# Kernel optimization log

Hardware: AMD Instinct MI355X
Metric: run time of the kernel (lower is better)

## Reference

```python
import jax, jax.numpy as jnp
import numpy as np

EMBED_DIM = 1024
NUM_HEADS = 16
HEAD_DIM = EMBED_DIM // NUM_HEADS
BATCH = 1
SEQ = 4096


def setup_inputs() -> dict:
    key = jax.random.key(0)
    ks = jax.random.split(key, 9)
    s = 1.0 / np.sqrt(EMBED_DIM)
    inp = {
        "x": jax.random.normal(ks[0], (BATCH, SEQ, EMBED_DIM), dtype=jnp.float32),
        "Wq": jax.random.uniform(ks[1], (EMBED_DIM, EMBED_DIM), jnp.float32, -s, s),
        "bq": jax.random.uniform(ks[2], (EMBED_DIM,), jnp.float32, -s, s),
        "Wk": jax.random.uniform(ks[3], (EMBED_DIM, EMBED_DIM), jnp.float32, -s, s),
        "bk": jax.random.uniform(ks[4], (EMBED_DIM,), jnp.float32, -s, s),
        "Wv": jax.random.uniform(ks[5], (EMBED_DIM, EMBED_DIM), jnp.float32, -s, s),
        "bv": jax.random.uniform(ks[6], (EMBED_DIM,), jnp.float32, -s, s),
        "Wo": jax.random.uniform(ks[7], (EMBED_DIM, EMBED_DIM), jnp.float32, -s, s),
        "bo": jax.random.uniform(ks[8], (EMBED_DIM,), jnp.float32, -s, s),
    }
    return inp


def _attention(x, Wq, bq, Wk, bk, Wv, bv, Wo, bo):
    B, S, E = x.shape
    # project and split heads: [B, H, S, D]
    def split_heads(t):
        return t.reshape(B, S, NUM_HEADS, HEAD_DIM).transpose(0, 2, 1, 3)
    q = split_heads(x @ Wq + bq)
    k = split_heads(x @ Wk + bk)
    v = split_heads(x @ Wv + bv)
    scale = 1.0 / np.sqrt(HEAD_DIM).astype(np.float32)
    # scores: [B, H, S, S] (torch code materializes these per query chunk;
    # math is identical computed in one shot)
    scores = jnp.einsum("bhqd,bhkd->bhqk", q, k) * scale
    attn = jax.nn.softmax(scores, axis=-1)  # dropout p=0 -> identity
    out = jnp.einsum("bhqk,bhkd->bhqd", attn, v)
    out = out.transpose(0, 2, 1, 3).reshape(B, S, E)
    return out @ Wo + bo


def reference(x, Wq, bq, Wk, bk, Wv, bv, Wo, bo):
    return _attention(x, Wq, bq, Wk, bk, Wv, bv, Wo, bo)
```

## Files before the change

kernel.cpp:

```cpp
#include <hip/hip_runtime.h>
#include <stdint.h>

typedef __bf16 bf16;
typedef __bf16 bf16x2 __attribute__((ext_vector_type(2)));
typedef __bf16 bf16x8 __attribute__((ext_vector_type(8)));
typedef float f32x4 __attribute__((ext_vector_type(4)));
typedef uint32_t u32x2 __attribute__((ext_vector_type(2)));

#define EMB 1024
#define SEQ 4096
#define NH 16
#define HD 64

__device__ __forceinline__ void glds16(const void* g, void* l) {
    __builtin_amdgcn_global_load_lds(
        (const __attribute__((address_space(1))) uint32_t*)(uintptr_t)g,
        (__attribute__((address_space(3))) uint32_t*)(uintptr_t)l,
        16, 0, 0);
}

union PU { bf16x2 h; uint32_t u; };
__device__ __forceinline__ uint32_t pack_bf16(float a, float b) {
    PU p; p.h = (bf16x2){(bf16)a, (bf16)b}; return p.u;
}

template<int NT>
__device__ __forceinline__ void transpose_tile(const float* in, bf16* out,
                                               int R, int C, int rbase, int cbase,
                                               bf16* tile ) {
    const int t = threadIdx.x;
    constexpr int PASSES = 512 / NT;
#pragma unroll
    for (int p = 0; p < PASSES; ++p) {
        int idx = t + p * NT;
        int r = idx >> 3;
        int seg = idx & 7;
        const float* src = in + (size_t)(rbase + r) * C + cbase + seg * 8;
        f32x4 a = *(const f32x4*)src;
        f32x4 b = *(const f32x4*)(src + 4);
#pragma unroll
        for (int i = 0; i < 4; ++i) {
            tile[r * 81 + seg * 8 + i]     = (bf16)a[i];
            tile[r * 81 + seg * 8 + 4 + i] = (bf16)b[i];
        }
    }
    __syncthreads();
#pragma unroll
    for (int p = 0; p < PASSES; ++p) {
        int idx = t + p * NT;
        int r = idx >> 3;
        int seg = idx & 7;
        bf16x8 v;
#pragma unroll
        for (int i = 0; i < 8; ++i) v[i] = tile[(seg * 8 + i) * 81 + r];
        *(bf16x8*)(out + (size_t)(cbase + r) * R + rbase + seg * 8) = v;
    }
}

__global__ __launch_bounds__(256) void prep_k(const float* __restrict__ W0,
                                              const float* __restrict__ W1,
                                              const float* __restrict__ W2,
                                              bf16* __restrict__ o0,
                                              bf16* __restrict__ o1,
                                              bf16* __restrict__ o2,
                                              const float* __restrict__ x,
                                              bf16* __restrict__ xb) {
    __shared__ bf16 tile[64 * 81];
    if (blockIdx.z < 3) {
        const float* in = blockIdx.z == 0 ? W0 : (blockIdx.z == 1 ? W1 : W2);
        bf16* out = blockIdx.z == 0 ? o0 : (blockIdx.z == 1 ? o1 : o2);
        transpose_tile<256>(in, out, EMB, EMB, blockIdx.y * 64, blockIdx.x * 64, tile);
    } else {
        size_t linear = blockIdx.y * 16 + blockIdx.x;
#pragma unroll
        for (int i = 0; i < 4; ++i) {
            size_t base = linear * 16384 + (size_t)i * 4096 + threadIdx.x * 16;
#pragma unroll
            for (int h = 0; h < 2; ++h) {
                f32x4 a = *(const f32x4*)(x + base + h * 8);
                f32x4 b = *(const f32x4*)(x + base + h * 8 + 4);
                bf16x8 v;
#pragma unroll
                for (int j = 0; j < 4; ++j) { v[j] = (bf16)a[j]; v[4 + j] = (bf16)b[j]; }
                *(bf16x8*)(xb + base + h * 8) = v;
            }
        }
    }
}

__global__ __launch_bounds__(256) void transpose_k(const float* __restrict__ in,
                                                   bf16* __restrict__ out,
                                                   int R, int C) {
    __shared__ bf16 tile[64 * 81];
    transpose_tile<256>(in, out, R, C, blockIdx.y * 64, blockIdx.x * 64, tile);
}

template<bool A_BF16, bool FUSED>
__global__ __launch_bounds__(256, 3) void gemm_m97(
    const void* __restrict__ A,
    const bf16* __restrict__ Wt0, const bf16* __restrict__ Wt1,
    const bf16* __restrict__ Wt2,
    const float* __restrict__ b0, const float* __restrict__ b1,
    const float* __restrict__ b2,
    void* __restrict__ out0, void* __restrict__ out1,
    bf16* __restrict__ outVt) {
    constexpr int SMEM_BYTES = A_BF16 ? (FUSED ? 18432 : 16384) : 24576;
    __shared__ __align__(16) uint8_t smem[SMEM_BYTES];
    float* aF = (float*)smem;
    bf16*  aB = (bf16*)smem;
    bf16*  bL = (bf16*)(smem + (A_BF16 ? 8192 : 16384));

    const int t = threadIdx.x;
    const int lane = t & 63;
    const int wave = t >> 6;
    const int l15 = lane & 15;
    const int quad = lane >> 4;
    const int wrow = (wave >> 1) * 64;
    const int wcol = (wave & 1) * 64;
    const int nb = blockIdx.x;
    const int which = FUSED ? (nb >> 3) : 0;
    const int ncol = (FUSED ? (nb & 7) : nb) * 128;
    const int mblock = blockIdx.y * 128;

    const bf16* Wt = FUSED ? (which == 0 ? Wt0 : (which == 1 ? Wt1 : Wt2)) : Wt0;
    const float* bias = FUSED ? (which == 0 ? b0 : (which == 1 ? b1 : b2)) : b0;

    float bv[4];
#pragma unroll
    for (int nt = 0; nt < 4; ++nt) bv[nt] = bias[ncol + wcol + nt * 16 + l15];

    f32x4 acc[4][4];
#pragma unroll
    for (int mt = 0; mt < 4; ++mt)
#pragma unroll
        for (int nt = 0; nt < 4; ++nt) acc[mt][nt] = (f32x4){0.f, 0.f, 0.f, 0.f};

    const int a4row = lane >> 3, a4seg = lane & 7;
    const int b2row = lane >> 2, b2seg = lane & 3;

    for (int k0 = 0; k0 < EMB; k0 += 32) {
        __syncthreads();
        if constexpr (!A_BF16) {
#pragma unroll
            for (int i = 0; i < 4; ++i) {
                int row = i * 32 + wave * 8 + a4row;
                int sg = a4seg ^ (row & 7);
                glds16((const float*)A + (size_t)(mblock + row) * EMB + k0 + sg * 4,
                       smem + i * 4096 + wave * 1024);
            }
        } else {
#pragma unroll
            for (int i = 0; i < 2; ++i) {
                int row = i * 64 + wave * 16 + b2row;
                int sg = b2seg ^ ((row >> 1) & 3);
                glds16((const bf16*)A + (size_t)(mblock + row) * EMB + k0 + sg * 8,
                       smem + i * 4096 + wave * 1024);
            }
        }
#pragma unroll
        for (int i = 0; i < 2; ++i) {
            int row = i * 64 + wave * 16 + b2row;
            int sg = b2seg ^ ((row >> 1) & 3);
            glds16(Wt + (size_t)(ncol + row) * EMB + k0 + sg * 8,
                   (uint8_t*)bL + i * 4096 + wave * 1024);
        }
        __syncthreads();

        bf16x8 af[4], bfr[4];
#pragma unroll
        for (int mt = 0; mt < 4; ++mt) {
            int rl = wrow + mt * 16 + l15;
            if constexpr (!A_BF16) {
                f32x4 lo = *(const f32x4*)(aF + rl * 32 + ((2 * quad)     ^ (rl & 7)) * 4);
                f32x4 hi = *(const f32x4*)(aF + rl * 32 + ((2 * quad + 1) ^ (rl & 7)) * 4);
#pragma unroll
                for (int j = 0; j < 4; ++j) {
                    af[mt][j]     = (bf16)lo[j];
                    af[mt][4 + j] = (bf16)hi[j];
                }
            } else {
                af[mt] = *(const bf16x8*)(aB + rl * 32 + (quad ^ ((rl >> 1) & 3)) * 8);
            }
        }
#pragma unroll
        for (int nt = 0; nt < 4; ++nt) {
            int rl = wcol + nt * 16 + l15;
            bfr[nt] = *(const bf16x8*)(bL + rl * 32 + (quad ^ ((rl >> 1) & 3)) * 8);
        }
#pragma unroll
        for (int mt = 0; mt < 4; ++mt)
#pragma unroll
            for (int nt = 0; nt < 4; ++nt)
                acc[mt][nt] = __builtin_amdgcn_mfma_f32_16x16x32_bf16(
                    af[mt], bfr[nt], acc[mt][nt], 0, 0, 0);
    }

    if (!FUSED || which < 2) {
        void* outp = FUSED ? (which == 0 ? out0 : out1) : out0;
#pragma unroll
        for (int mt = 0; mt < 4; ++mt)
#pragma unroll
            for (int nt = 0; nt < 4; ++nt)
#pragma unroll
                for (int r = 0; r < 4; ++r) {
                    size_t row = mblock + wrow + mt * 16 + quad * 4 + r;
                    size_t col = ncol + wcol + nt * 16 + l15;
                    float v = acc[mt][nt][r] + bv[nt];
                    if constexpr (FUSED) ((bf16*)outp)[row * EMB + col] = (bf16)v;
                    else                 ((float*)outp)[row * EMB + col] = v;
                }
    } else if constexpr (FUSED) {
        __syncthreads();
        bf16* tr = (bf16*)smem + wave * 2304;
#pragma unroll
        for (int ch = 0; ch < 2; ++ch) {
#pragma unroll
            for (int mt = 0; mt < 4; ++mt)
#pragma unroll
                for (int ntl = 0; ntl < 2; ++ntl)
#pragma unroll
                    for (int r = 0; r < 4; ++r) {
                        int d_local = ntl * 16 + l15;
                        int s_local = mt * 16 + quad * 4 + r;
                        int nt = 2 * ch + ntl;
                        tr[d_local * 72 + s_local] = (bf16)(acc[mt][nt][r] + bv[nt]);
                    }
            int d2 = lane & 31, h2 = lane >> 5;
#pragma unroll
            for (int j = 0; j < 4; ++j) {
                bf16x8 v = *(const bf16x8*)(tr + d2 * 72 + h2 * 32 + j * 8);
                *(bf16x8*)(outVt + (size_t)(ncol + wcol + ch * 32 + d2) * SEQ +
                           mblock + wrow + h2 * 32 + j * 8) = v;
            }
        }
    }
}

__global__ __launch_bounds__(256, 2) void attn_k(bf16* __restrict__ QO,
                                                 const bf16* __restrict__ Km,
                                                 const bf16* __restrict__ Vt,
                                                 const float* __restrict__ Wo,
                                                 bf16* __restrict__ wt_o) {
    __shared__ bf16 k_lds[2][64 * 64];
    __shared__ bf16 v_lds[2][64 * 64];
    __shared__ bf16 p_lds[4][2][16][72];

    if (blockIdx.y == NH) {
        bf16* tile = &k_lds[0][0];
#pragma unroll 1
        for (int i = 0; i < 8; ++i) {
            int tid = blockIdx.x * 8 + i;
            int ty = tid >> 4, tx = tid & 15;
            transpose_tile<256>(Wo, wt_o, EMB, EMB, ty * 64, tx * 64, tile);
            __syncthreads();
        }
        return;
    }

    const int t = threadIdx.x;
    const int lane = t & 63;
    const int wave = t >> 6;
    const int l15 = lane & 15;
    const int quad = lane >> 4;
    const int sw = l15 & 7;
    const int h = blockIdx.y;
    const int qbase = blockIdx.x * 128 + wave * 32;
    const float QSCALE = 0.125f * 1.4426950408889634f;

    const int srow = wave * 16 + (lane >> 3);
    const int ssg  = lane & 7;

    bf16x8 qf[2][2];
#pragma unroll
    for (int qt = 0; qt < 2; ++qt)
#pragma unroll
        for (int kk = 0; kk < 2; ++kk) {
            bf16x8 raw = *(const bf16x8*)(QO + (size_t)(qbase + qt * 16 + l15) * EMB +
                                          h * HD + kk * 32 + quad * 8);
#pragma unroll
            for (int j = 0; j < 8; ++j) qf[qt][kk][j] = (bf16)((float)raw[j] * QSCALE);
        }

    f32x4 o_acc[2][4];
#pragma unroll
    for (int qt = 0; qt < 2; ++qt)
#pragma unroll
        for (int c = 0; c < 4; ++c) o_acc[qt][c] = (f32x4){0.f, 0.f, 0.f, 0.f};
    float l_run[2] = {0.f, 0.f};

#define STAGE(buf, kbv)                                                               \
    do {                                                                              \
        _Pragma("unroll")                                                             \
        for (int i = 0; i < 2; ++i) {                                                 \
            int rr = srow + i * 8;                                                    \
            int sg = ssg ^ (rr & 7);                                                  \
            glds16(Km + (size_t)((kbv) + rr) * EMB + h * HD + sg * 8,                 \
                   &k_lds[buf][(wave * 16 + i * 8) * 64]);                            \
            glds16(Vt + (size_t)(h * HD + rr) * SEQ + (kbv) + sg * 8,                 \
                   &v_lds[buf][(wave * 16 + i * 8) * 64]);                            \
        }                                                                             \
    } while (0)

#define COMPUTE(buf)                                                                  \
    do {                                                                              \
        f32x4 s[2][4];                                                                \
        _Pragma("unroll")                                                             \
        for (int c = 0; c < 4; ++c) {                                                 \
            int row = c * 16 + l15;                                                   \
            bf16x8 k0 = *(const bf16x8*)&k_lds[buf][row * 64 + ((quad)     ^ sw) * 8];\
            bf16x8 k1 = *(const bf16x8*)&k_lds[buf][row * 64 + ((4 + quad) ^ sw) * 8];\
            _Pragma("unroll")                                                         \
            for (int qt = 0; qt < 2; ++qt) {                                          \
                f32x4 z = (f32x4){0.f, 0.f, 0.f, 0.f};                                \
                z = __builtin_amdgcn_mfma_f32_16x16x32_bf16(k0, qf[qt][0], z, 0, 0, 0);\
                s[qt][c] = __builtin_amdgcn_mfma_f32_16x16x32_bf16(k1, qf[qt][1], z, 0, 0, 0);\
            }                                                                         \
        }                                                                             \
        _Pragma("unroll")                                                             \
        for (int qt = 0; qt < 2; ++qt)                                                \
            _Pragma("unroll")                                                         \
            for (int c = 0; c < 4; ++c) {                                             \
                float p0 = __builtin_amdgcn_exp2f(s[qt][c][0]);                       \
                float p1 = __builtin_amdgcn_exp2f(s[qt][c][1]);                       \
                float p2 = __builtin_amdgcn_exp2f(s[qt][c][2]);                       \
                float p3 = __builtin_amdgcn_exp2f(s[qt][c][3]);                       \
                l_run[qt] += (p0 + p1) + (p2 + p3);                                   \
                *(u32x2*)&p_lds[wave][qt][l15][c * 16 + quad * 4] =                   \
                    (u32x2){pack_bf16(p0, p1), pack_bf16(p2, p3)};                    \
            }                                                                         \
        bf16x8 pf[2][2];                                                              \
        _Pragma("unroll")                                                             \
        for (int qt = 0; qt < 2; ++qt)                                                \
            _Pragma("unroll")                                                         \
            for (int tt = 0; tt < 2; ++tt)                                            \
                pf[qt][tt] = *(const bf16x8*)&p_lds[wave][qt][l15][tt * 32 + quad * 8];\
        _Pragma("unroll")                                                             \
        for (int c = 0; c < 4; ++c) {                                                 \
            int row = c * 16 + l15;                                                   \
            bf16x8 v0 = *(const bf16x8*)&v_lds[buf][row * 64 + ((quad)     ^ sw) * 8];\
            bf16x8 v1 = *(const bf16x8*)&v_lds[buf][row * 64 + ((4 + quad) ^ sw) * 8];\
            _Pragma("unroll")                                                         \
            for (int qt = 0; qt < 2; ++qt) {                                          \
                o_acc[qt][c] = __builtin_amdgcn_mfma_f32_16x16x32_bf16(               \
                    pf[qt][0], v0, o_acc[qt][c], 0, 0, 0);                            \
                o_acc[qt][c] = __builtin_amdgcn_mfma_f32_16x16x32_bf16(               \
                    pf[qt][1], v1, o_acc[qt][c], 0, 0, 0);                            \
            }                                                                         \
        }                                                                             \
    } while (0)

    STAGE(0, 0);
    for (int kb = 0; kb < SEQ; kb += 128) {
        __syncthreads();
        STAGE(1, kb + 64);
        COMPUTE(0);
        __syncthreads();
        if (kb + 128 < SEQ) STAGE(0, kb + 128);
        COMPUTE(1);
    }
#undef STAGE
#undef COMPUTE

#pragma unroll
    for (int qt = 0; qt < 2; ++qt) {
        float l = l_run[qt];
        l += __shfl_xor(l, 16);
        l += __shfl_xor(l, 32);
        float inv = 1.0f / l;
#pragma unroll
        for (int r = 0; r < 4; ++r) {
            float invr = __shfl(inv, quad * 4 + r);
#pragma unroll
            for (int c = 0; c < 4; ++c)
                QO[(size_t)(qbase + qt * 16 + quad * 4 + r) * EMB + h * HD + c * 16 + l15] =
                    (bf16)(o_acc[qt][c][r] * invr);
        }
    }
}

extern "C" void kernel_launch(void* const* d_in, const int* in_sizes, int n_in,
                              void* d_out, int out_size, void* d_ws, size_t ws_size,
                              hipStream_t stream) {
    const float* x  = (const float*)d_in[0];
    const float* Wq = (const float*)d_in[1];
    const float* bq = (const float*)d_in[2];
    const float* Wk = (const float*)d_in[3];
    const float* bk = (const float*)d_in[4];
    const float* Wv = (const float*)d_in[5];
    const float* bv = (const float*)d_in[6];
    const float* Wo = (const float*)d_in[7];
    const float* bo = (const float*)d_in[8];

    const size_t MAT = (size_t)SEQ * EMB;
    const size_t WMT = (size_t)EMB * EMB;

    bf16* o16   = (bf16*)d_out;
    bf16* Wt_q  = o16;
    bf16* Wt_k  = o16 + WMT;
    bf16* Wt_v  = o16 + 2 * WMT;
    bf16* Vtb   = o16 + 3 * WMT;

    bf16* wsb   = (bf16*)d_ws;
    bf16* QOb   = wsb;
    bf16* Kb    = wsb + MAT;
    bf16* xb    = wsb + 2 * MAT;

    dim3 blk(256);
    dim3 gP(16, 16, 4);
    dim3 gF(24, SEQ / 128);
    dim3 gO(EMB / 128, SEQ / 128);

    if (ws_size >= 3 * MAT * sizeof(bf16)) {
        prep_k<<<gP, blk, 0, stream>>>(Wq, Wk, Wv, Wt_q, Wt_k, Wt_v, x, xb);

        gemm_m97<true, true><<<gF, blk, 0, stream>>>(
            xb, Wt_q, Wt_k, Wt_v, bq, bk, bv, QOb, Kb, Vtb);

        dim3 gA(SEQ / 128, NH + 1);
        attn_k<<<gA, blk, 0, stream>>>(QOb, Kb, Vtb, Wo, xb);

        gemm_m97<true, false><<<gO, blk, 0, stream>>>(
            QOb, xb, nullptr, nullptr, bo, nullptr, nullptr, d_out, nullptr, nullptr);
    } else {
        bf16* Wt_o = wsb + MAT;
        dim3 gTW(EMB / 64, EMB / 64);
        transpose_k<<<gTW, blk, 0, stream>>>(Wq, Wt_q, EMB, EMB);
        transpose_k<<<gTW, blk, 0, stream>>>(Wk, Wt_k, EMB, EMB);
        transpose_k<<<gTW, blk, 0, stream>>>(Wv, Wt_v, EMB, EMB);
        gemm_m97<false, true><<<gF, blk, 0, stream>>>(
            x, Wt_q, Wt_k, Wt_v, bq, bk, bv, QOb, Kb, Vtb);
        dim3 gA(SEQ / 128, NH);
        attn_k<<<gA, blk, 0, stream>>>(QOb, Kb, Vtb, nullptr, nullptr);
        transpose_k<<<gTW, blk, 0, stream>>>(Wo, Wt_o, EMB, EMB);
        gemm_m97<true, false><<<gO, blk, 0, stream>>>(
            QOb, Wt_o, nullptr, nullptr, bo, nullptr, nullptr, d_out, nullptr, nullptr);
    }
}
```

Before: 234.1 us.

## Switch attention to 32x32x16 MFMA and keep P in registers via permlane32 swap

Replaces the 16x16x32 MFMA tiling in the attention kernel with 32x32x16 MFMAs, computing S^T per 32-key block so the probability fragments can be reshuffled in registers with permlane32_swap instead of round-tripping through a per-wave LDS buffer. This removes the p_lds shared array and its store/load traffic and raises the occupancy hint from 2 to 3 blocks per CU. The output normalization and store are rewritten for the 32x32 accumulator layout. Register pressure from f32x16 accumulators may limit whether the higher occupancy target is reachable.

Result: no change. 232.1 us (-0.9%).

```diff
diff --git a/kernel.cpp b/kernel.cpp
--- a/kernel.cpp
+++ b/kernel.cpp
@@ -5,6 +5,7 @@
 typedef __bf16 bf16x2 __attribute__((ext_vector_type(2)));
 typedef __bf16 bf16x8 __attribute__((ext_vector_type(8)));
 typedef float f32x4 __attribute__((ext_vector_type(4)));
+typedef float f32x16 __attribute__((ext_vector_type(16)));
 typedef uint32_t u32x2 __attribute__((ext_vector_type(2)));
 
 #define EMB 1024
@@ -23,6 +24,7 @@
 __device__ __forceinline__ uint32_t pack_bf16(float a, float b) {
     PU p; p.h = (bf16x2){(bf16)a, (bf16)b}; return p.u;
 }
+union FU { bf16x8 v; uint32_t u[4]; };
 
 template<int NT>
 __device__ __forceinline__ void transpose_tile(const float* in, bf16* out,
@@ -236,14 +238,13 @@
     }
 }
 
-__global__ __launch_bounds__(256, 2) void attn_k(bf16* __restrict__ QO,
+__global__ __launch_bounds__(256, 3) void attn_k(bf16* __restrict__ QO,
                                                  const bf16* __restrict__ Km,
                                                  const bf16* __restrict__ Vt,
                                                  const float* __restrict__ Wo,
                                                  bf16* __restrict__ wt_o) {
     __shared__ bf16 k_lds[2][64 * 64];
     __shared__ bf16 v_lds[2][64 * 64];
-    __shared__ bf16 p_lds[4][2][16][72];
 
     if (blockIdx.y == NH) {
         bf16* tile = &k_lds[0][0];
@@ -260,33 +261,31 @@
     const int t = threadIdx.x;
     const int lane = t & 63;
     const int wave = t >> 6;
-    const int l15 = lane & 15;
-    const int quad = lane >> 4;
-    const int sw = l15 & 7;
-    const int h = blockIdx.y;
+    const int l31 = lane & 31;
+    const int hi = lane >> 5;
+    const int l7 = lane & 7;
+    const int head = blockIdx.y;
     const int qbase = blockIdx.x * 128 + wave * 32;
     const float QSCALE = 0.125f * 1.4426950408889634f;
 
     const int srow = wave * 16 + (lane >> 3);
     const int ssg  = lane & 7;
 
-    bf16x8 qf[2][2];
-#pragma unroll
-    for (int qt = 0; qt < 2; ++qt)
-#pragma unroll
-        for (int kk = 0; kk < 2; ++kk) {
-            bf16x8 raw = *(const bf16x8*)(QO + (size_t)(qbase + qt * 16 + l15) * EMB +
-                                          h * HD + kk * 32 + quad * 8);
-#pragma unroll
-            for (int j = 0; j < 8; ++j) qf[qt][kk][j] = (bf16)((float)raw[j] * QSCALE);
-        }
-
-    f32x4 o_acc[2][4];
-#pragma unroll
-    for (int qt = 0; qt < 2; ++qt)
-#pragma unroll
-        for (int c = 0; c < 4; ++c) o_acc[qt][c] = (f32x4){0.f, 0.f, 0.f, 0.f};
-    float l_run[2] = {0.f, 0.f};
+    bf16x8 qf[4];
+#pragma unroll
+    for (int s = 0; s < 4; ++s) {
+        bf16x8 raw = *(const bf16x8*)(QO + (size_t)(qbase + l31) * EMB +
+                                      head * HD + s * 16 + hi * 8);
+#pragma unroll
+        for (int j = 0; j < 8; ++j) qf[s][j] = (bf16)((float)raw[j] * QSCALE);
+    }
+
+    f32x16 o_acc[2];
+#pragma unroll
+    for (int db = 0; db < 2; ++db)
+#pragma unroll
+        for (int z = 0; z < 16; ++z) o_acc[db][z] = 0.f;
+    float l_run = 0.f;
 
 #define STAGE(buf, kbv)                                                               \
     do {                                                                              \
@@ -294,57 +293,51 @@
         for (int i = 0; i < 2; ++i) {                                                 \
             int rr = srow + i * 8;                                                    \
             int sg = ssg ^ (rr & 7);                                                  \
-            glds16(Km + (size_t)((kbv) + rr) * EMB + h * HD + sg * 8,                 \
+            glds16(Km + (size_t)((kbv) + rr) * EMB + head * HD + sg * 8,              \
                    &k_lds[buf][(wave * 16 + i * 8) * 64]);                            \
-            glds16(Vt + (size_t)(h * HD + rr) * SEQ + (kbv) + sg * 8,                 \
+            glds16(Vt + (size_t)(head * HD + rr) * SEQ + (kbv) + sg * 8,              \
                    &v_lds[buf][(wave * 16 + i * 8) * 64]);                            \
         }                                                                             \
     } while (0)
 
 #define COMPUTE(buf)                                                                  \
     do {                                                                              \
-        f32x4 s[2][4];                                                                \
         _Pragma("unroll")                                                             \
-        for (int c = 0; c < 4; ++c) {                                                 \
-            int row = c * 16 + l15;                                                   \
-            bf16x8 k0 = *(const bf16x8*)&k_lds[buf][row * 64 + ((quad)     ^ sw) * 8];\
-            bf16x8 k1 = *(const bf16x8*)&k_lds[buf][row * 64 + ((4 + quad) ^ sw) * 8];\
+        for (int b = 0; b < 2; ++b) {                                                 \
+            f32x16 sa;                                                               \
             _Pragma("unroll")                                                         \
-            for (int qt = 0; qt < 2; ++qt) {                                          \
-                f32x4 z = (f32x4){0.f, 0.f, 0.f, 0.f};                                \
-                z = __builtin_amdgcn_mfma_f32_16x16x32_bf16(k0, qf[qt][0], z, 0, 0, 0);\
-                s[qt][c] = __builtin_amdgcn_mfma_f32_16x16x32_bf16(k1, qf[qt][1], z, 0, 0, 0);\
+            for (int z = 0; z < 16; ++z) sa[z] = 0.f;                                 \
+            _Pragma("unroll")                                                         \
+            for (int s = 0; s < 4; ++s) {                                             \
+                bf16x8 kf = *(const bf16x8*)&k_lds[buf][(32 * b + l31) * 64 +         \
+                                (((2 * s + hi) ^ l7) * 8)];                           \
+                sa = __builtin_amdgcn_mfma_f32_32x32x16_bf16(kf, qf[s], sa, 0, 0, 0); \
             }                                                                         \
-        }                                                                             \
-        _Pragma("unroll")                                                             \
-        for (int qt = 0; qt < 2; ++qt)                                                \
+            uint32_t u0[4], u1[4];                                                    \
             _Pragma("unroll")                                                         \
-            for (int c = 0; c < 4; ++c) {                                             \
-                float p0 = __builtin_amdgcn_exp2f(s[qt][c][0]);                       \
-                float p1 = __builtin_amdgcn_exp2f(s[qt][c][1]);                       \
-                float p2 = __builtin_amdgcn_exp2f(s[qt][c][2]);                       \
-                float p3 = __builtin_amdgcn_exp2f(s[qt][c][3]);                       \
-                l_run[qt] += (p0 + p1) + (p2 + p3);                                   \
-                *(u32x2*)&p_lds[wave][qt][l15][c * 16 + quad * 4] =                   \
-                    (u32x2){pack_bf16(p0, p1), pack_bf16(p2, p3)};                    \
+            for (int i = 0; i < 4; ++i) {                                             \
+                float p0 = __builtin_amdgcn_exp2f(sa[4 * i + 0]);                     \
+                float p1 = __builtin_amdgcn_exp2f(sa[4 * i + 1]);                     \
+                float p2 = __builtin_amdgcn_exp2f(sa[4 * i + 2]);                     \
+                float p3 = __builtin_amdgcn_exp2f(sa[4 * i + 3]);                     \
+                l_run += (p0 + p1) + (p2 + p3);                                       \
+                u0[i] = pack_bf16(p0, p1);                                            \
+                u1[i] = pack_bf16(p2, p3);                                            \
             }                                                                         \
-        bf16x8 pf[2][2];                                                              \
-        _Pragma("unroll")                                                             \
-        for (int qt = 0; qt < 2; ++qt)                                                \
             _Pragma("unroll")                                                         \
-            for (int tt = 0; tt < 2; ++tt)                                            \
-                pf[qt][tt] = *(const bf16x8*)&p_lds[wave][qt][l15][tt * 32 + quad * 8];\
-        _Pragma("unroll")                                                             \
-        for (int c = 0; c < 4; ++c) {                                                 \
-            int row = c * 16 + l15;                                                   \
-            bf16x8 v0 = *(const bf16x8*)&v_lds[buf][row * 64 + ((quad)     ^ sw) * 8];\
-            bf16x8 v1 = *(const bf16x8*)&v_lds[buf][row * 64 + ((4 + quad) ^ sw) * 8];\
-            _Pragma("unroll")                                                         \
-            for (int qt = 0; qt < 2; ++qt) {                                          \
-                o_acc[qt][c] = __builtin_amdgcn_mfma_f32_16x16x32_bf16(               \
-                    pf[qt][0], v0, o_acc[qt][c], 0, 0, 0);                            \
-                o_acc[qt][c] = __builtin_amdgcn_mfma_f32_16x16x32_bf16(               \
-                    pf[qt][1], v1, o_acc[qt][c], 0, 0, 0);                            \
+            for (int sp = 0; sp < 2; ++sp) {                                          \
+                u32x2 ra = __builtin_amdgcn_permlane32_swap(u0[2 * sp], u0[2 * sp + 1], false, false); \
+                u32x2 rb = __builtin_amdgcn_permlane32_swap(u1[2 * sp], u1[2 * sp + 1], false, false); \
+                FU A;                                                                 \
+                A.u[0] = ra[0]; A.u[1] = rb[0]; A.u[2] = ra[1]; A.u[3] = rb[1];       \
+                int tt = 2 * b + sp;                                                  \
+                _Pragma("unroll")                                                     \
+                for (int db = 0; db < 2; ++db) {                                      \
+                    bf16x8 vf = *(const bf16x8*)&v_lds[buf][(db * 32 + l31) * 64 +    \
+                                    (((2 * tt + hi) ^ l7) * 8)];                      \
+                    o_acc[db] = __builtin_amdgcn_mfma_f32_32x32x16_bf16(              \
+                        A.v, vf, o_acc[db], 0, 0, 0);                                 \
+                }                                                                     \
             }                                                                         \
         }                                                                             \
     } while (0)
@@ -361,21 +354,20 @@
 #undef STAGE
 #undef COMPUTE
 
-#pragma unroll
-    for (int qt = 0; qt < 2; ++qt) {
-        float l = l_run[qt];
-        l += __shfl_xor(l, 16);
-        l += __shfl_xor(l, 32);
-        float inv = 1.0f / l;
-#pragma unroll
-        for (int r = 0; r < 4; ++r) {
-            float invr = __shfl(inv, quad * 4 + r);
-#pragma unroll
-            for (int c = 0; c < 4; ++c)
-                QO[(size_t)(qbase + qt * 16 + quad * 4 + r) * EMB + h * HD + c * 16 + l15] =
-                    (bf16)(o_acc[qt][c][r] * invr);
-        }
-    }
+    l_run += __shfl_xor(l_run, 32);
+    float inv = 1.0f / l_run;
+    float invr[16];
+#pragma unroll
+    for (int reg = 0; reg < 16; ++reg)
+        invr[reg] = __shfl(inv, (reg & 3) + 8 * (reg >> 2) + 4 * hi);
+#pragma unroll
+    for (int db = 0; db < 2; ++db)
+#pragma unroll
+        for (int reg = 0; reg < 16; ++reg) {
+            int q = (reg & 3) + 8 * (reg >> 2) + 4 * hi;
+            QO[(size_t)(qbase + q) * EMB + head * HD + db * 32 + l31] =
+                (bf16)(o_acc[db][reg] * invr[reg]);
+        }
 }
 
 extern "C" void kernel_launch(void* const* d_in, const int* in_sizes, int n_in,
```
